# Kernel optimization log

Hardware: AMD Instinct MI355X
Metric: run time of the kernel (lower is better)

Reference implementation:

```python
import jax, jax.numpy as jnp
import numpy as np

B, S, D = 2, 2048, 4096
NH, NKV, HD = 32, 8, 128
N_REP = NH // NKV
MAX_B, MAX_S = 2, 2048


def _rope(x, cos, sin):
    # x: [b, s, h, hd]; cos/sin: [s, hd//2]
    xr = x.reshape(*x.shape[:-1], HD // 2, 2)
    xe, xo = xr[..., 0], xr[..., 1]
    c = cos[None, :, None, :]
    s = sin[None, :, None, :]
    oe = xe * c - xo * s
    oo = xe * s + xo * c
    return jnp.stack([oe, oo], axis=-1).reshape(x.shape)


def setup_inputs() -> dict:
    key = jax.random.key(0)
    ks = jax.random.split(key, 8)
    x = jax.random.normal(ks[0], (B, S, D), dtype=jnp.float32)
    # xavier-normal-ish weights (module uses identity init_method, i.e. uninitialized;
    # we use scaled gaussians for a well-conditioned reference)
    wq = jax.random.normal(ks[1], (NH * HD, D), dtype=jnp.float32) * (1.0 / np.sqrt(D))
    wk = jax.random.normal(ks[2], (NKV * HD, D), dtype=jnp.float32) * (1.0 / np.sqrt(D))
    wv = jax.random.normal(ks[3], (NKV * HD, D), dtype=jnp.float32) * (1.0 / np.sqrt(D))
    wo = jax.random.normal(ks[4], (D, NH * HD), dtype=jnp.float32) * (1.0 / np.sqrt(D))
    # rotary freqs (llama-style, theta=500000)
    theta = 500000.0
    inv = 1.0 / (theta ** (np.arange(0, HD, 2, dtype=np.float32) / HD))  # [hd/2]
    t = np.arange(S, dtype=np.float32)
    ang = np.outer(t, inv)  # [S, hd/2]
    freqs_cos = jnp.asarray(np.cos(ang), dtype=jnp.float32)
    freqs_sin = jnp.asarray(np.sin(ang), dtype=jnp.float32)
    # causal mask
    mask = jnp.where(jnp.tril(jnp.ones((S, S), dtype=bool)), 0.0, -jnp.inf).astype(jnp.float32)
    cache_k = jnp.zeros((MAX_B, MAX_S, NKV, HD), dtype=jnp.float32)
    cache_v = jnp.zeros((MAX_B, MAX_S, NKV, HD), dtype=jnp.float32)
    return {"x": x, "wq": wq, "wk": wk, "wv": wv, "wo": wo,
            "freqs_cos": freqs_cos, "freqs_sin": freqs_sin,
            "mask": mask, "cache_k": cache_k, "cache_v": cache_v,
            "start_pos": 0}


def reference(x, wq, wk, wv, wo, freqs_cos, freqs_sin, mask, cache_k, cache_v, start_pos):
    bsz, seqlen, _ = x.shape
    xq = jnp.einsum('bsd,qd->bsq', x, wq).reshape(bsz, seqlen, NH, HD)
    xk = jnp.einsum('bsd,kd->bsk', x, wk).reshape(bsz, seqlen, NKV, HD)
    xv = jnp.einsum('bsd,vd->bsv', x, wv).reshape(bsz, seqlen, NKV, HD)
    xq = _rope(xq, freqs_cos, freqs_sin)
    xk = _rope(xk, freqs_cos, freqs_sin)
    # KV-cache update then read back valid prefix
    cache_k = jax.lax.dynamic_update_slice(cache_k, xk, (0, start_pos, 0, 0))
    cache_v = jax.lax.dynamic_update_slice(cache_v, xv, (0, start_pos, 0, 0))
    kvlen = start_pos + seqlen
    keys = cache_k[:bsz, :kvlen]    # [b, T, nkv, hd]
    values = cache_v[:bsz, :kvlen]
    # GQA repeat_kv
    keys = jnp.broadcast_to(keys[:, :, :, None, :], (bsz, kvlen, NKV, N_REP, HD)).reshape(bsz, kvlen, NH, HD)
    values = jnp.broadcast_to(values[:, :, :, None, :], (bsz, kvlen, NKV, N_REP, HD)).reshape(bsz, kvlen, NH, HD)
    scores = jnp.einsum('bqhd,bkhd->bhqk', xq, keys) / np.sqrt(HD)
    scores = scores + mask[None, None, :, :]
    probs = jax.nn.softmax(scores, axis=-1)
    out = jnp.einsum('bhqk,bkhd->bqhd', probs, values).reshape(bsz, seqlen, NH * HD)
    return jnp.einsum('bsq,dq->bsd', out, wo)
```

## Files before the change

kernel.cpp:

```cpp
#include <hip/hip_runtime.h>
#include <hip/hip_bf16.h>

#define B_ 2
#define S_ 2048
#define D_ 4096
#define NH_ 32
#define NKV_ 8
#define HD_ 128
#define M_ (B_ * S_)

typedef __bf16 bf16x8_t __attribute__((ext_vector_type(8)));
typedef float f32x4_t __attribute__((ext_vector_type(4)));

__device__ __forceinline__ void gload16(const __bf16* g, __bf16* l) {
  __builtin_amdgcn_global_load_lds(
      (const __attribute__((address_space(1))) void*)g,
      (__attribute__((address_space(3))) void*)l, 16, 0, 0);
}

__global__ __launch_bounds__(256) void convert_main(const float* __restrict__ x,
                                                    const float* __restrict__ wq,
                                                    const float* __restrict__ wk,
                                                    const float* __restrict__ wv,
                                                    __bf16* __restrict__ xb,
                                                    __bf16* __restrict__ wqkv) {
  size_t c = (size_t)blockIdx.x * 256 + threadIdx.x;
  const float* src;
  __bf16* dst;
  if (c < 2097152) { src = x + c * 8; dst = xb + c * 8; }
  else if (c < 4194304) { c -= 2097152; src = wq + c * 8; dst = wqkv + c * 8; }
  else if (c < 4718592) { c -= 4194304; src = wk + c * 8; dst = wqkv + 16777216 + c * 8; }
  else { c -= 4718592; src = wv + c * 8; dst = wqkv + 20971520 + c * 8; }
  const float4* s4 = reinterpret_cast<const float4*>(src);
  float4 a = s4[0], b = s4[1];
  bf16x8_t t;
  t[0] = (__bf16)a.x; t[1] = (__bf16)a.y; t[2] = (__bf16)a.z; t[3] = (__bf16)a.w;
  t[4] = (__bf16)b.x; t[5] = (__bf16)b.y; t[6] = (__bf16)b.z; t[7] = (__bf16)b.w;
  *reinterpret_cast<bf16x8_t*>(dst) = t;
}

__global__ __launch_bounds__(256) void convert_wo(const float* __restrict__ wo,
                                                  __bf16* __restrict__ wob) {
  size_t c = (size_t)blockIdx.x * 256 + threadIdx.x;
  const float4* s4 = reinterpret_cast<const float4*>(wo + c * 8);
  float4 a = s4[0], b = s4[1];
  bf16x8_t t;
  t[0] = (__bf16)a.x; t[1] = (__bf16)a.y; t[2] = (__bf16)a.z; t[3] = (__bf16)a.w;
  t[4] = (__bf16)b.x; t[5] = (__bf16)b.y; t[6] = (__bf16)b.z; t[7] = (__bf16)b.w;
  *reinterpret_cast<bf16x8_t*>(wob + c * 8) = t;
}

template <bool SPLIT, bool OUTF32>
__global__ __launch_bounds__(256) void gemm_bt(const __bf16* __restrict__ A,
                                               const __bf16* __restrict__ Bm,
                                               void* __restrict__ C0,
                                               void* __restrict__ C1,
                                               int N, int K) {
  __shared__ __attribute__((aligned(16))) __bf16 As[128 * 32];
  __shared__ __attribute__((aligned(16))) __bf16 Bs[128 * 32];
  const int tid = threadIdx.x;
  const int lane = tid & 63;
  const int w = tid >> 6;
  const int lo = lane & 15;
  const int hi = lane >> 4;
  const int wm = (w & 1) * 64;
  const int wn = (w >> 1) * 64;
  const int m0 = blockIdx.y * 128;
  const int n0 = blockIdx.x * 128;

  const int srow = w * 32 + (lane >> 2);
  const int scol = (lane & 3) * 8;
  const __bf16* ga0 = A + (size_t)(m0 + srow) * K + scol;
  const __bf16* ga1 = A + (size_t)(m0 + srow + 16) * K + scol;
  const __bf16* gb0 = Bm + (size_t)(n0 + srow) * K + scol;
  const __bf16* gb1 = Bm + (size_t)(n0 + srow + 16) * K + scol;
  __bf16* la0 = &As[(w * 32) * 32];
  __bf16* la1 = &As[(w * 32 + 16) * 32];
  __bf16* lb0 = &Bs[(w * 32) * 32];
  __bf16* lb1 = &Bs[(w * 32 + 16) * 32];

  f32x4_t acc[4][4] = {};

  for (int k0 = 0; k0 < K; k0 += 32) {
    __syncthreads();
    gload16(ga0 + k0, la0);
    gload16(ga1 + k0, la1);
    gload16(gb0 + k0, lb0);
    gload16(gb1 + k0, lb1);
    __syncthreads();
    bf16x8_t af[4], bfr[4];
#pragma unroll
    for (int mi = 0; mi < 4; mi++)
      af[mi] = *reinterpret_cast<const bf16x8_t*>(&As[(wm + mi * 16 + lo) * 32 + hi * 8]);
#pragma unroll
    for (int ni = 0; ni < 4; ni++)
      bfr[ni] = *reinterpret_cast<const bf16x8_t*>(&Bs[(wn + ni * 16 + lo) * 32 + hi * 8]);
#pragma unroll
    for (int mi = 0; mi < 4; mi++)
#pragma unroll
      for (int ni = 0; ni < 4; ni++)
        acc[mi][ni] = __builtin_amdgcn_mfma_f32_16x16x32_bf16(af[mi], bfr[ni], acc[mi][ni], 0, 0, 0);
  }

  __bf16* Cb = nullptr;
  float* Cf = nullptr;
  int ldc, nb;
  if constexpr (SPLIT) {
    if (n0 < 4096) { Cb = (__bf16*)C0; ldc = 4096; nb = n0; }
    else { Cb = (__bf16*)C1; ldc = 2048; nb = n0 - 4096; }
  } else {
    ldc = N; nb = n0;
    if constexpr (OUTF32) Cf = (float*)C0; else Cb = (__bf16*)C0;
  }
#pragma unroll
  for (int mi = 0; mi < 4; mi++) {
    const int mrow = m0 + wm + mi * 16 + hi * 4;
#pragma unroll
    for (int ni = 0; ni < 4; ni++) {
      const int ncol = nb + wn + ni * 16 + lo;
#pragma unroll
      for (int r = 0; r < 4; r++) {
        if constexpr (OUTF32)
          Cf[(size_t)(mrow + r) * ldc + ncol] = acc[mi][ni][r];
        else
          Cb[(size_t)(mrow + r) * ldc + ncol] = (__bf16)acc[mi][ni][r];
      }
    }
  }
}

typedef __bf16 bf16x2_t __attribute__((ext_vector_type(2)));
__global__ __launch_bounds__(256) void rope_kernel(__bf16* __restrict__ q,
                                                   __bf16* __restrict__ kv,
                                                   const float* __restrict__ fcos,
                                                   const float* __restrict__ fsin) {
  const int p = blockIdx.x * 256 + threadIdx.x;
  const int j = p & 63;
  int rem = p >> 6;
  const int hh = rem % (NH_ + NKV_);
  rem /= (NH_ + NKV_);
  const int s = rem % S_;
  const int b = rem / S_;
  const float c = fcos[s * 64 + j];
  const float sn = fsin[s * 64 + j];
  __bf16* base;
  if (hh < NH_)
    base = q + ((size_t)(b * S_ + s) * NH_ + hh) * HD_ + 2 * j;
  else
    base = kv + (size_t)(b * S_ + s) * 2048 + (hh - NH_) * HD_ + 2 * j;
  bf16x2_t xv = *reinterpret_cast<const bf16x2_t*>(base);
  const float xe = (float)xv[0], xo = (float)xv[1];
  bf16x2_t ov;
  ov[0] = (__bf16)(xe * c - xo * sn);
  ov[1] = (__bf16)(xe * sn + xo * c);
  *reinterpret_cast<bf16x2_t*>(base) = ov;
}

__global__ __launch_bounds__(256) void attn_kernel(const __bf16* __restrict__ q,
                                                   const __bf16* __restrict__ kv,
                                                   __bf16* __restrict__ o) {
  const int qt = blockIdx.x;
  const int h = blockIdx.y;
  const int b = blockIdx.z;
  const int hkv = h >> 2;
  const int tid = threadIdx.x;
  const int lane = tid & 63;
  const int w = tid >> 6;
  const int lo = lane & 15;
  const int hi = lane >> 4;
  const int q0 = qt * 128;

  __shared__ __attribute__((aligned(16))) __bf16 Ks[64 * 132];
  __shared__ __attribute__((aligned(16))) __bf16 Vt[128 * 68];
  __shared__ __attribute__((aligned(16))) __bf16 Ps[4][32 * 68];

  bf16x8_t qf[2][4];
#pragma unroll
  for (int mi = 0; mi < 2; mi++) {
    const size_t qbase = ((size_t)(b * S_ + q0 + w * 32 + mi * 16 + lo) * NH_ + h) * HD_;
#pragma unroll
    for (int ks = 0; ks < 4; ks++)
      qf[mi][ks] = *reinterpret_cast<const bf16x8_t*>(q + qbase + ks * 32 + hi * 8);
  }

  f32x4_t o_acc[2][8] = {};
  f32x4_t l_acc[2] = {};
  float m_prev[2][4];
#pragma unroll
  for (int mi = 0; mi < 2; mi++)
#pragma unroll
    for (int r = 0; r < 4; r++) m_prev[mi][r] = -1e30f;

  bf16x8_t ones;
#pragma unroll
  for (int e = 0; e < 8; e++) ones[e] = (__bf16)1.0f;

  constexpr float SC = 0.08838834764831845f * 1.44269504088896f;

  const int nkt = qt * 2 + 2;
  for (int kt = 0; kt < nkt; kt++) {
    const int kt0 = kt * 64;
    __syncthreads();
#pragma unroll
    for (int i = 0; i < 4; i++) {
      const int c = tid + i * 256;
      const int key = c >> 4, hc = c & 15;
      *reinterpret_cast<bf16x8_t*>(&Ks[key * 132 + hc * 8]) =
          *reinterpret_cast<const bf16x8_t*>(kv + (size_t)(b * S_ + kt0 + key) * 2048 + hkv * 128 + hc * 8);
    }
#pragma unroll
    for (int i = 0; i < 4; i++) {
      const int c = tid + i * 256;
      const int key = c & 63, hc = c >> 6;
      bf16x8_t vv = *reinterpret_cast<const bf16x8_t*>(
          kv + (size_t)(b * S_ + kt0 + key) * 2048 + 1024 + hkv * 128 + hc * 8);
#pragma unroll
      for (int e = 0; e < 8; e++) Vt[(hc * 8 + e) * 68 + key] = vv[e];
    }
    __syncthreads();

    f32x4_t s_acc[2][4] = {};
#pragma unroll
    for (int ks = 0; ks < 4; ks++) {
      bf16x8_t kf[4];
#pragma unroll
      for (int t = 0; t < 4; t++)
        kf[t] = *reinterpret_cast<const bf16x8_t*>(&Ks[(t * 16 + lo) * 132 + ks * 32 + hi * 8]);
#pragma unroll
      for (int mi = 0; mi < 2; mi++)
#pragma unroll
        for (int t = 0; t < 4; t++)
          s_acc[mi][t] = __builtin_amdgcn_mfma_f32_16x16x32_bf16(qf[mi][ks], kf[t], s_acc[mi][t], 0, 0, 0);
    }

#pragma unroll
    for (int mi = 0; mi < 2; mi++) {
      const int rowbase = q0 + w * 32 + mi * 16;
      const bool need_mask = (kt0 + 63) > rowbase;
      float sv[4][4];
#pragma unroll
      for (int t = 0; t < 4; t++)
#pragma unroll
        for (int r = 0; r < 4; r++) {
          float val = s_acc[mi][t][r] * SC;
          if (need_mask && (kt0 + t * 16 + lo) > (rowbase + hi * 4 + r)) val = -1e30f;
          sv[t][r] = val;
        }
      float alpha[4], mnew[4];
#pragma unroll
      for (int r = 0; r < 4; r++) {
        float mx = fmaxf(fmaxf(sv[0][r], sv[1][r]), fmaxf(sv[2][r], sv[3][r]));
#pragma unroll
        for (int off = 1; off < 16; off <<= 1) mx = fmaxf(mx, __shfl_xor(mx, off));
        mnew[r] = fmaxf(m_prev[mi][r], mx);
        alpha[r] = __builtin_amdgcn_exp2f(m_prev[mi][r] - mnew[r]);
        m_prev[mi][r] = mnew[r];
      }
#pragma unroll
      for (int t = 0; t < 4; t++)
#pragma unroll
        for (int r = 0; r < 4; r++)
          Ps[w][(mi * 16 + hi * 4 + r) * 68 + t * 16 + lo] =
              (__bf16)__builtin_amdgcn_exp2f(sv[t][r] - mnew[r]);
#pragma unroll
      for (int t8 = 0; t8 < 8; t8++)
#pragma unroll
        for (int r = 0; r < 4; r++) o_acc[mi][t8][r] *= alpha[r];
#pragma unroll
      for (int r = 0; r < 4; r++) l_acc[mi][r] *= alpha[r];
    }

#pragma unroll
    for (int ks2 = 0; ks2 < 2; ks2++) {
      bf16x8_t pf[2];
#pragma unroll
      for (int mi = 0; mi < 2; mi++)
        pf[mi] = *reinterpret_cast<const bf16x8_t*>(&Ps[w][(mi * 16 + lo) * 68 + ks2 * 32 + hi * 8]);
#pragma unroll
      for (int mi = 0; mi < 2; mi++)
        l_acc[mi] = __builtin_amdgcn_mfma_f32_16x16x32_bf16(pf[mi], ones, l_acc[mi], 0, 0, 0);
#pragma unroll
      for (int t8 = 0; t8 < 8; t8++) {
        bf16x8_t vf = *reinterpret_cast<const bf16x8_t*>(&Vt[(t8 * 16 + lo) * 68 + ks2 * 32 + hi * 8]);
#pragma unroll
        for (int mi = 0; mi < 2; mi++)
          o_acc[mi][t8] = __builtin_amdgcn_mfma_f32_16x16x32_bf16(pf[mi], vf, o_acc[mi][t8], 0, 0, 0);
      }
    }
  }

#pragma unroll
  for (int mi = 0; mi < 2; mi++)
#pragma unroll
    for (int r = 0; r < 4; r++) {
      const float inv = 1.0f / l_acc[mi][r];
      const int qr = q0 + w * 32 + mi * 16 + hi * 4 + r;
      const size_t obase = ((size_t)(b * S_ + qr) * NH_ + h) * HD_;
#pragma unroll
      for (int t8 = 0; t8 < 8; t8++)
        o[obase + t8 * 16 + lo] = (__bf16)(o_acc[mi][t8][r] * inv);
    }
}

extern "C" void kernel_launch(void* const* d_in, const int* in_sizes, int n_in,
                              void* d_out, int out_size, void* d_ws, size_t ws_size,
                              hipStream_t stream) {
  const float* x = (const float*)d_in[0];
  const float* wq = (const float*)d_in[1];
  const float* wk = (const float*)d_in[2];
  const float* wv = (const float*)d_in[3];
  const float* wo = (const float*)d_in[4];
  const float* fcos = (const float*)d_in[5];
  const float* fsin = (const float*)d_in[6];
  float* out = (float*)d_out;

  __bf16* xb   = (__bf16*)d_ws;
  __bf16* wqkv = xb + (size_t)16777216;
  __bf16* qb   = (__bf16*)d_ws + (size_t)41943040;
  __bf16* kvb  = qb + (size_t)16777216;
  __bf16* wob  = xb;
  __bf16* ab   = wqkv;

  convert_main<<<20480, 256, 0, stream>>>(x, wq, wk, wv, xb, wqkv);
  gemm_bt<true, false><<<dim3(48, 32), 256, 0, stream>>>(xb, wqkv, qb, kvb, 6144, D_);
  convert_wo<<<8192, 256, 0, stream>>>(wo, wob);
  rope_kernel<<<(M_ * (NH_ + NKV_) * (HD_ / 2)) / 256, 256, 0, stream>>>(qb, kvb, fcos, fsin);
  attn_kernel<<<dim3(S_ / 128, NH_, B_), 256, 0, stream>>>(qb, kvb, ab);
  gemm_bt<false, true><<<dim3(32, 32), 256, 0, stream>>>(ab, wob, out, nullptr, D_, D_);
}
```

Measured before the change: 1.105 ms.

## Pair causal query tiles per block, prefetch KV into registers, raise MFMA priority

Each attention block now handles two query tiles, qt and 15-qt, so every block does the same amount of causal work and the grid halves. Block indices are remapped so that blocks sharing a KV head sit next to each other in launch order, which should improve L2 reuse. The next K/V tile is loaded into registers while the current tile is being computed, overlapping global loads with MFMA work. s_setprio is raised around the MFMA sections. The cost is higher register pressure from the prefetch buffers and only 512 blocks, which may not fill every CU.

```diff
diff --git a/kernel.cpp b/kernel.cpp
--- a/kernel.cpp
+++ b/kernel.cpp
@@ -159,147 +159,175 @@
 __global__ __launch_bounds__(256) void attn_kernel(const __bf16* __restrict__ q,
                                                    const __bf16* __restrict__ kv,
                                                    __bf16* __restrict__ o) {
-  const int qt = blockIdx.x;
-  const int h = blockIdx.y;
-  const int b = blockIdx.z;
-  const int hkv = h >> 2;
+  const int flat = blockIdx.x + (blockIdx.y << 3) + (blockIdx.z << 8);
+  const int hkv = flat & 7;
+  const int idx = flat >> 3;
+  const int h = hkv * 4 + ((idx >> 3) & 3);
+  const int b = idx >> 5;
+  const int xpair = idx & 7;
+
   const int tid = threadIdx.x;
   const int lane = tid & 63;
   const int w = tid >> 6;
   const int lo = lane & 15;
   const int hi = lane >> 4;
-  const int q0 = qt * 128;
 
   __shared__ __attribute__((aligned(16))) __bf16 Ks[64 * 132];
   __shared__ __attribute__((aligned(16))) __bf16 Vt[128 * 68];
   __shared__ __attribute__((aligned(16))) __bf16 Ps[4][32 * 68];
 
-  bf16x8_t qf[2][4];
-#pragma unroll
-  for (int mi = 0; mi < 2; mi++) {
-    const size_t qbase = ((size_t)(b * S_ + q0 + w * 32 + mi * 16 + lo) * NH_ + h) * HD_;
-#pragma unroll
-    for (int ks = 0; ks < 4; ks++)
-      qf[mi][ks] = *reinterpret_cast<const bf16x8_t*>(q + qbase + ks * 32 + hi * 8);
-  }
-
-  f32x4_t o_acc[2][8] = {};
-  f32x4_t l_acc[2] = {};
-  float m_prev[2][4];
-#pragma unroll
-  for (int mi = 0; mi < 2; mi++)
-#pragma unroll
-    for (int r = 0; r < 4; r++) m_prev[mi][r] = -1e30f;
-
   bf16x8_t ones;
 #pragma unroll
   for (int e = 0; e < 8; e++) ones[e] = (__bf16)1.0f;
 
   constexpr float SC = 0.08838834764831845f * 1.44269504088896f;
 
-  const int nkt = qt * 2 + 2;
-  for (int kt = 0; kt < nkt; kt++) {
-    const int kt0 = kt * 64;
-    __syncthreads();
+  const __bf16* kvb = kv + (size_t)b * S_ * 2048 + hkv * 128;
+  int kkey[4], khc[4], vkey[4], vhc[4];
+#pragma unroll
+  for (int i = 0; i < 4; i++) {
+    const int c = tid + i * 256;
+    kkey[i] = c >> 4; khc[i] = c & 15;
+    vkey[i] = c & 63; vhc[i] = c >> 6;
+  }
+
+  bf16x8_t kreg[4], vreg[4];
+
+  for (int pass = 0; pass < 2; pass++) {
+    const int qt = pass ? (15 - xpair) : xpair;
+    const int q0 = qt * 128;
+
+    bf16x8_t qf[2][4];
+#pragma unroll
+    for (int mi = 0; mi < 2; mi++) {
+      const size_t qbase = ((size_t)(b * S_ + q0 + w * 32 + mi * 16 + lo) * NH_ + h) * HD_;
+#pragma unroll
+      for (int ks = 0; ks < 4; ks++)
+        qf[mi][ks] = *reinterpret_cast<const bf16x8_t*>(q + qbase + ks * 32 + hi * 8);
+    }
+
+    f32x4_t o_acc[2][8] = {};
+    f32x4_t l_acc[2] = {};
+    float m_prev[2][4];
+#pragma unroll
+    for (int mi = 0; mi < 2; mi++)
+#pragma unroll
+      for (int r = 0; r < 4; r++) m_prev[mi][r] = -1e30f;
+
+    const int nkt = qt * 2 + 2;
+
 #pragma unroll
     for (int i = 0; i < 4; i++) {
-      const int c = tid + i * 256;
-      const int key = c >> 4, hc = c & 15;
-      *reinterpret_cast<bf16x8_t*>(&Ks[key * 132 + hc * 8]) =
-          *reinterpret_cast<const bf16x8_t*>(kv + (size_t)(b * S_ + kt0 + key) * 2048 + hkv * 128 + hc * 8);
+      kreg[i] = *reinterpret_cast<const bf16x8_t*>(kvb + (size_t)kkey[i] * 2048 + khc[i] * 8);
+      vreg[i] = *reinterpret_cast<const bf16x8_t*>(kvb + (size_t)vkey[i] * 2048 + 1024 + vhc[i] * 8);
     }
-#pragma unroll
-    for (int i = 0; i < 4; i++) {
-      const int c = tid + i * 256;
-      const int key = c & 63, hc = c >> 6;
-      bf16x8_t vv = *reinterpret_cast<const bf16x8_t*>(
-          kv + (size_t)(b * S_ + kt0 + key) * 2048 + 1024 + hkv * 128 + hc * 8);
-#pragma unroll
-      for (int e = 0; e < 8; e++) Vt[(hc * 8 + e) * 68 + key] = vv[e];
+
+    for (int kt = 0; kt < nkt; kt++) {
+      const int kt0 = kt * 64;
+      __syncthreads();
+#pragma unroll
+      for (int i = 0; i < 4; i++)
+        *reinterpret_cast<bf16x8_t*>(&Ks[kkey[i] * 132 + khc[i] * 8]) = kreg[i];
+#pragma unroll
+      for (int i = 0; i < 4; i++)
+#pragma unroll
+        for (int e = 0; e < 8; e++) Vt[(vhc[i] * 8 + e) * 68 + vkey[i]] = vreg[i][e];
+      __syncthreads();
+      if (kt + 1 < nkt) {
+        const int nt0 = (kt + 1) * 64;
+#pragma unroll
+        for (int i = 0; i < 4; i++) {
+          kreg[i] = *reinterpret_cast<const bf16x8_t*>(kvb + (size_t)(nt0 + kkey[i]) * 2048 + khc[i] * 8);
+          vreg[i] = *reinterpret_cast<const bf16x8_t*>(kvb + (size_t)(nt0 + vkey[i]) * 2048 + 1024 + vhc[i] * 8);
+        }
+      }
+
+      f32x4_t s_acc[2][4] = {};
+      __builtin_amdgcn_s_setprio(1);
+#pragma unroll
+      for (int ks = 0; ks < 4; ks++) {
+        bf16x8_t kf[4];
+#pragma unroll
+        for (int t = 0; t < 4; t++)
+          kf[t] = *reinterpret_cast<const bf16x8_t*>(&Ks[(t * 16 + lo) * 132 + ks * 32 + hi * 8]);
+#pragma unroll
+        for (int mi = 0; mi < 2; mi++)
+#pragma unroll
+          for (int t = 0; t < 4; t++)
+            s_acc[mi][t] = __builtin_amdgcn_mfma_f32_16x16x32_bf16(qf[mi][ks], kf[t], s_acc[mi][t], 0, 0, 0);
+      }
+      __builtin_amdgcn_s_setprio(0);
+
+#pragma unroll
+      for (int mi = 0; mi < 2; mi++) {
+        const int rowbase = q0 + w * 32 + mi * 16;
+        const bool need_mask = (kt0 + 63) > rowbase;
+        float sv[4][4];
+#pragma unroll
+        for (int t = 0; t < 4; t++)
+#pragma unroll
+          for (int r = 0; r < 4; r++) {
+            float val = s_acc[mi][t][r] * SC;
+            if (need_mask && (kt0 + t * 16 + lo) > (rowbase + hi * 4 + r)) val = -1e30f;
+            sv[t][r] = val;
+          }
+        float alpha[4], mnew[4];
+#pragma unroll
+        for (int r = 0; r < 4; r++) {
+          float mx = fmaxf(fmaxf(sv[0][r], sv[1][r]), fmaxf(sv[2][r], sv[3][r]));
+#pragma unroll
+          for (int off = 1; off < 16; off <<= 1) mx = fmaxf(mx, __shfl_xor(mx, off));
+          mnew[r] = fmaxf(m_prev[mi][r], mx);
+          alpha[r] = __builtin_amdgcn_exp2f(m_prev[mi][r] - mnew[r]);
+          m_prev[mi][r] = mnew[r];
+        }
+#pragma unroll
+        for (int t = 0; t < 4; t++)
+#pragma unroll
+          for (int r = 0; r < 4; r++)
+            Ps[w][(mi * 16 + hi * 4 + r) * 68 + t * 16 + lo] =
+                (__bf16)__builtin_amdgcn_exp2f(sv[t][r] - mnew[r]);
+#pragma unroll
+        for (int t8 = 0; t8 < 8; t8++)
+#pragma unroll
+          for (int r = 0; r < 4; r++) o_acc[mi][t8][r] *= alpha[r];
+#pragma unroll
+        for (int r = 0; r < 4; r++) l_acc[mi][r] *= alpha[r];
+      }
+
+      __builtin_amdgcn_s_setprio(1);
+#pragma unroll
+      for (int ks2 = 0; ks2 < 2; ks2++) {
+        bf16x8_t pf[2];
+#pragma unroll
+        for (int mi = 0; mi < 2; mi++)
+          pf[mi] = *reinterpret_cast<const bf16x8_t*>(&Ps[w][(mi * 16 + lo) * 68 + ks2 * 32 + hi * 8]);
+#pragma unroll
+        for (int mi = 0; mi < 2; mi++)
+          l_acc[mi] = __builtin_amdgcn_mfma_f32_16x16x32_bf16(pf[mi], ones, l_acc[mi], 0, 0, 0);
+#pragma unroll
+        for (int t8 = 0; t8 < 8; t8++) {
+          bf16x8_t vf = *reinterpret_cast<const bf16x8_t*>(&Vt[(t8 * 16 + lo) * 68 + ks2 * 32 + hi * 8]);
+#pragma unroll
+          for (int mi = 0; mi < 2; mi++)
+            o_acc[mi][t8] = __builtin_amdgcn_mfma_f32_16x16x32_bf16(pf[mi], vf, o_acc[mi][t8], 0, 0, 0);
+        }
+      }
+      __builtin_amdgcn_s_setprio(0);
     }
-    __syncthreads();
-
-    f32x4_t s_acc[2][4] = {};
-#pragma unroll
-    for (int ks = 0; ks < 4; ks++) {
-      bf16x8_t kf[4];
-#pragma unroll
-      for (int t = 0; t < 4; t++)
-        kf[t] = *reinterpret_cast<const bf16x8_t*>(&Ks[(t * 16 + lo) * 132 + ks * 32 + hi * 8]);
-#pragma unroll
-      for (int mi = 0; mi < 2; mi++)
-#pragma unroll
-        for (int t = 0; t < 4; t++)
-          s_acc[mi][t] = __builtin_amdgcn_mfma_f32_16x16x32_bf16(qf[mi][ks], kf[t], s_acc[mi][t], 0, 0, 0);
-    }
-
-#pragma unroll
-    for (int mi = 0; mi < 2; mi++) {
-      const int rowbase = q0 + w * 32 + mi * 16;
-      const bool need_mask = (kt0 + 63) > rowbase;
-      float sv[4][4];
-#pragma unroll
-      for (int t = 0; t < 4; t++)
-#pragma unroll
-        for (int r = 0; r < 4; r++) {
-          float val = s_acc[mi][t][r] * SC;
-          if (need_mask && (kt0 + t * 16 + lo) > (rowbase + hi * 4 + r)) val = -1e30f;
-          sv[t][r] = val;
-        }
-      float alpha[4], mnew[4];
+
+#pragma unroll
+    for (int mi = 0; mi < 2; mi++)
 #pragma unroll
       for (int r = 0; r < 4; r++) {
-        float mx = fmaxf(fmaxf(sv[0][r], sv[1][r]), fmaxf(sv[2][r], sv[3][r]));
-#pragma unroll
-        for (int off = 1; off < 16; off <<= 1) mx = fmaxf(mx, __shfl_xor(mx, off));
-        mnew[r] = fmaxf(m_prev[mi][r], mx);
-        alpha[r] = __builtin_amdgcn_exp2f(m_prev[mi][r] - mnew[r]);
-        m_prev[mi][r] = mnew[r];
-      }
-#pragma unroll
-      for (int t = 0; t < 4; t++)
-#pragma unroll
-        for (int r = 0; r < 4; r++)
-          Ps[w][(mi * 16 + hi * 4 + r) * 68 + t * 16 + lo] =
-              (__bf16)__builtin_amdgcn_exp2f(sv[t][r] - mnew[r]);
-#pragma unroll
-      for (int t8 = 0; t8 < 8; t8++)
-#pragma unroll
-        for (int r = 0; r < 4; r++) o_acc[mi][t8][r] *= alpha[r];
-#pragma unroll
-      for (int r = 0; r < 4; r++) l_acc[mi][r] *= alpha[r];
-    }
-
-#pragma unroll
-    for (int ks2 = 0; ks2 < 2; ks2++) {
-      bf16x8_t pf[2];
-#pragma unroll
-      for (int mi = 0; mi < 2; mi++)
-        pf[mi] = *reinterpret_cast<const bf16x8_t*>(&Ps[w][(mi * 16 + lo) * 68 + ks2 * 32 + hi * 8]);
-#pragma unroll
-      for (int mi = 0; mi < 2; mi++)
-        l_acc[mi] = __builtin_amdgcn_mfma_f32_16x16x32_bf16(pf[mi], ones, l_acc[mi], 0, 0, 0);
-#pragma unroll
-      for (int t8 = 0; t8 < 8; t8++) {
-        bf16x8_t vf = *reinterpret_cast<const bf16x8_t*>(&Vt[(t8 * 16 + lo) * 68 + ks2 * 32 + hi * 8]);
-#pragma unroll
-        for (int mi = 0; mi < 2; mi++)
-          o_acc[mi][t8] = __builtin_amdgcn_mfma_f32_16x16x32_bf16(pf[mi], vf, o_acc[mi][t8], 0, 0, 0);
-      }
-    }
-  }
-
-#pragma unroll
-  for (int mi = 0; mi < 2; mi++)
-#pragma unroll
-    for (int r = 0; r < 4; r++) {
-      const float inv = 1.0f / l_acc[mi][r];
-      const int qr = q0 + w * 32 + mi * 16 + hi * 4 + r;
-      const size_t obase = ((size_t)(b * S_ + qr) * NH_ + h) * HD_;
-#pragma unroll
-      for (int t8 = 0; t8 < 8; t8++)
-        o[obase + t8 * 16 + lo] = (__bf16)(o_acc[mi][t8][r] * inv);
-    }
+        const float inv = 1.0f / l_acc[mi][r];
+        const int qr = q0 + w * 32 + mi * 16 + hi * 4 + r;
+        const size_t obase = ((size_t)(b * S_ + qr) * NH_ + h) * HD_;
+#pragma unroll
+        for (int t8 = 0; t8 < 8; t8++)
+          o[obase + t8 * 16 + lo] = (__bf16)(o_acc[mi][t8][r] * inv);
+      }
+  }
 }
 
 extern "C" void kernel_launch(void* const* d_in, const int* in_sizes, int n_in,
@@ -325,6 +353,6 @@
   gemm_bt<true, false><<<dim3(48, 32), 256, 0, stream>>>(xb, wqkv, qb, kvb, 6144, D_);
   convert_wo<<<8192, 256, 0, stream>>>(wo, wob);
   rope_kernel<<<(M_ * (NH_ + NKV_) * (HD_ / 2)) / 256, 256, 0, stream>>>(qb, kvb, fcos, fsin);
-  attn_kernel<<<dim3(S_ / 128, NH_, B_), 256, 0, stream>>>(qb, kvb, ab);
+  attn_kernel<<<dim3(8, NH_, B_), 256, 0, stream>>>(qb, kvb, ab);
   gemm_bt<false, true><<<dim3(32, 32), 256, 0, stream>>>(ab, wob, out, nullptr, D_, D_);
 }
```

Measured after the change: 991.3 us. 1.11x faster.
